# Kernel optimization log

Measured on AMD Instinct MI355X. Metric: run time of the kernel, lower is better.

The kernel has to match this reference:

```python
import jax, jax.numpy as jnp
import numpy as np

NTAPS = 63
BATCH = 32
SAMPLES = 2_097_152


def setup_inputs() -> dict:
    key = jax.random.key(0)
    k1, k2, k3, k4 = jax.random.split(key, 4)
    x = jax.random.normal(k1, (BATCH, 1, SAMPLES), dtype=jnp.float32)
    b = jax.random.normal(k2, (BATCH, NTAPS), dtype=jnp.float32)
    # adaptor: torch.nn.Linear(63, 63) -> weight (out,in), bias (out,)
    W = jax.random.normal(k3, (NTAPS, NTAPS), dtype=jnp.float32) * (1.0 / np.sqrt(NTAPS))
    bias = jax.random.normal(k4, (NTAPS,), dtype=jnp.float32) * (1.0 / np.sqrt(NTAPS))
    return {"x": x, "b": b, "W": W, "bias": bias}


def reference(x, b, W, bias):
    # x: (bs, 1, s); b: (bs, ntaps)
    bs, ch, s = x.shape
    # adaptor: Linear on filter coefficients
    b = b @ W.T + bias                      # (bs, ntaps)
    ntaps = b.shape[-1]
    pad = ntaps // 2
    # same-length FIR (torch conv1d = cross-correlation)
    xp = jnp.pad(x, ((0, 0), (0, 0), (pad, pad)))   # (bs, 1, s + 2*pad)
    # batched per-sample filters via grouped conv: batch dim -> channel groups
    lhs = xp.reshape(1, bs * ch, -1)        # N=1, C=bs
    rhs = b.reshape(bs, 1, ntaps)           # O=bs, I=1, taps
    y = jax.lax.conv_general_dilated(
        lhs, rhs,
        window_strides=(1,),
        padding="VALID",
        dimension_numbers=("NCH", "OIH", "NCH"),
        feature_group_count=bs,
    )                                       # (1, bs, s)
    return y.reshape(bs, ch, s)
```

## Files before the change

### kernel.cpp

```cpp
#include <hip/hip_runtime.h>

#define NTAPS   63
#define PAD     31
#define NBATCH  32
#define SAMPLES 2097152
#define ROUT    16
#define BLOCK   256
#define CHUNK   (ROUT * BLOCK)
#define WN      80

__global__ void filt_kernel(const float* __restrict__ b,
                            const float* __restrict__ W,
                            const float* __restrict__ bias,
                            float* __restrict__ filt) {
    const int batch = blockIdx.x;
    const int t = threadIdx.x;
    if (t < NTAPS) {
        const float* br = b + batch * NTAPS;
        const float* wr = W + t * NTAPS;
        float s = bias[t];
#pragma unroll
        for (int k = 0; k < NTAPS; ++k) s = fmaf(br[k], wr[k], s);
        filt[batch * NTAPS + t] = s;
    }
}

__global__ __launch_bounds__(BLOCK) void fir_kernel(const float* __restrict__ x,
                                                    const float* __restrict__ filt,
                                                    float* __restrict__ y) {
    const int batch = blockIdx.y;
    const int s0 = blockIdx.x * CHUNK + threadIdx.x * ROUT;
    const float* __restrict__ xb = x + (size_t)batch * SAMPLES;
    float*       __restrict__ yb = y + (size_t)batch * SAMPLES;
    const float* __restrict__ bf = filt + batch * NTAPS;

    float w[WN];
    const int base = s0 - 32;

    if (blockIdx.x != 0 && blockIdx.x != gridDim.x - 1) {
#pragma unroll
        for (int j = 0; j < WN / 4; ++j) {
            const float4 v = *reinterpret_cast<const float4*>(xb + base + 4 * j);
            w[4 * j + 0] = v.x;
            w[4 * j + 1] = v.y;
            w[4 * j + 2] = v.z;
            w[4 * j + 3] = v.w;
        }
    } else {
#pragma unroll
        for (int j = 0; j < WN / 4; ++j) {
            const int i = base + 4 * j;
            if (i >= 0 && i + 4 <= SAMPLES) {
                const float4 v = *reinterpret_cast<const float4*>(xb + i);
                w[4 * j + 0] = v.x;
                w[4 * j + 1] = v.y;
                w[4 * j + 2] = v.z;
                w[4 * j + 3] = v.w;
            } else {
#pragma unroll
                for (int e = 0; e < 4; ++e) {
                    const int ii = i + e;
                    w[4 * j + e] = (ii >= 0 && ii < SAMPLES) ? xb[ii] : 0.0f;
                }
            }
        }
    }

    float acc[ROUT];
#pragma unroll
    for (int r = 0; r < ROUT; ++r) acc[r] = 0.0f;

#pragma unroll
    for (int t = 0; t < NTAPS; ++t) {
        const float c = bf[t];
#pragma unroll
        for (int r = 0; r < ROUT; ++r) acc[r] = fmaf(c, w[r + t + 1], acc[r]);
    }

#pragma unroll
    for (int j = 0; j < ROUT / 4; ++j) {
        float4 v;
        v.x = acc[4 * j + 0];
        v.y = acc[4 * j + 1];
        v.z = acc[4 * j + 2];
        v.w = acc[4 * j + 3];
        *reinterpret_cast<float4*>(yb + s0 + 4 * j) = v;
    }
}

extern "C" void kernel_launch(void* const* d_in, const int* in_sizes, int n_in,
                              void* d_out, int out_size, void* d_ws, size_t ws_size,
                              hipStream_t stream) {
    const float* x    = (const float*)d_in[0];
    const float* b    = (const float*)d_in[1];
    const float* W    = (const float*)d_in[2];
    const float* bias = (const float*)d_in[3];
    float* y = (float*)d_out;
    float* filt = (float*)d_ws;

    filt_kernel<<<dim3(NBATCH), dim3(64), 0, stream>>>(b, W, bias, filt);

    dim3 grid(SAMPLES / CHUNK, NBATCH);
    fir_kernel<<<grid, dim3(BLOCK), 0, stream>>>(x, filt, y);
}
```

Measured before the change: 499.7 us.

## Stage input chunk through padded LDS tile with coalesced loads

Each block now loads its contiguous input chunk plus halo into shared memory using coalesced float4 loads, then each thread reads its 80-sample window from LDS. The previous version had each thread issue strided, overlapping float4 global loads for its window, which are uncoalesced across the wavefront and read the halo redundantly. LDS slots are padded by one float4 every four to avoid bank conflicts on the strided per-thread reads. The cost is a block-wide barrier and extra LDS usage, which may limit occupancy.

```diff
diff --git a/kernel.cpp b/kernel.cpp
--- a/kernel.cpp
+++ b/kernel.cpp
@@ -1,13 +1,15 @@
 #include <hip/hip_runtime.h>
 
 #define NTAPS   63
-#define PAD     31
 #define NBATCH  32
 #define SAMPLES 2097152
 #define ROUT    16
 #define BLOCK   256
 #define CHUNK   (ROUT * BLOCK)
-#define WN      80
+#define TILE_F  (CHUNK + 64)
+#define TILE_B  (TILE_F / 4)
+#define PSLOT(o) ((o) + ((o) >> 2))
+#define LDS_B   (PSLOT(TILE_B - 1) + 1)
 
 __global__ void filt_kernel(const float* __restrict__ b,
                             const float* __restrict__ W,
@@ -28,42 +30,53 @@
 __global__ __launch_bounds__(BLOCK) void fir_kernel(const float* __restrict__ x,
                                                     const float* __restrict__ filt,
                                                     float* __restrict__ y) {
+    __shared__ float4 tile[LDS_B];
+
+    const int tid = threadIdx.x;
     const int batch = blockIdx.y;
-    const int s0 = blockIdx.x * CHUNK + threadIdx.x * ROUT;
+    const int chunk0 = blockIdx.x * CHUNK;
     const float* __restrict__ xb = x + (size_t)batch * SAMPLES;
     float*       __restrict__ yb = y + (size_t)batch * SAMPLES;
     const float* __restrict__ bf = filt + batch * NTAPS;
 
-    float w[WN];
-    const int base = s0 - 32;
-
-    if (blockIdx.x != 0 && blockIdx.x != gridDim.x - 1) {
+    const bool interior = (blockIdx.x != 0) && (blockIdx.x != gridDim.x - 1);
+    if (interior) {
 #pragma unroll
-        for (int j = 0; j < WN / 4; ++j) {
-            const float4 v = *reinterpret_cast<const float4*>(xb + base + 4 * j);
-            w[4 * j + 0] = v.x;
-            w[4 * j + 1] = v.y;
-            w[4 * j + 2] = v.z;
-            w[4 * j + 3] = v.w;
+        for (int r = 0; r < 4; ++r) {
+            const int o = r * BLOCK + tid;
+            const float4 v = *reinterpret_cast<const float4*>(xb + chunk0 - 32 + 4 * o);
+            tile[PSLOT(o)] = v;
+        }
+        if (tid < TILE_B - 4 * BLOCK) {
+            const int o = 4 * BLOCK + tid;
+            const float4 v = *reinterpret_cast<const float4*>(xb + chunk0 - 32 + 4 * o);
+            tile[PSLOT(o)] = v;
         }
     } else {
 #pragma unroll
-        for (int j = 0; j < WN / 4; ++j) {
-            const int i = base + 4 * j;
-            if (i >= 0 && i + 4 <= SAMPLES) {
-                const float4 v = *reinterpret_cast<const float4*>(xb + i);
-                w[4 * j + 0] = v.x;
-                w[4 * j + 1] = v.y;
-                w[4 * j + 2] = v.z;
-                w[4 * j + 3] = v.w;
-            } else {
-#pragma unroll
-                for (int e = 0; e < 4; ++e) {
-                    const int ii = i + e;
-                    w[4 * j + e] = (ii >= 0 && ii < SAMPLES) ? xb[ii] : 0.0f;
-                }
+        for (int r = 0; r < 5; ++r) {
+            const int o = r * BLOCK + tid;
+            if (o < TILE_B) {
+                const int gi = chunk0 - 32 + 4 * o;
+                float4 v;
+                v.x = (gi + 0 >= 0 && gi + 0 < SAMPLES) ? xb[gi + 0] : 0.0f;
+                v.y = (gi + 1 >= 0 && gi + 1 < SAMPLES) ? xb[gi + 1] : 0.0f;
+                v.z = (gi + 2 >= 0 && gi + 2 < SAMPLES) ? xb[gi + 2] : 0.0f;
+                v.w = (gi + 3 >= 0 && gi + 3 < SAMPLES) ? xb[gi + 3] : 0.0f;
+                tile[PSLOT(o)] = v;
             }
         }
+    }
+    __syncthreads();
+
+    float w[80];
+#pragma unroll
+    for (int j = 0; j < 20; ++j) {
+        const float4 v = tile[5 * tid + j + (j >> 2)];
+        w[4 * j + 0] = v.x;
+        w[4 * j + 1] = v.y;
+        w[4 * j + 2] = v.z;
+        w[4 * j + 3] = v.w;
     }
 
     float acc[ROUT];
@@ -77,6 +90,7 @@
         for (int r = 0; r < ROUT; ++r) acc[r] = fmaf(c, w[r + t + 1], acc[r]);
     }
 
+    const int s0 = chunk0 + tid * ROUT;
 #pragma unroll
     for (int j = 0; j < ROUT / 4; ++j) {
         float4 v;
```

Result: faster. 448.8 us (-10.2%).
